# Kernel optimization log

Hardware: AMD Instinct MI355X
Metric: run time of the kernel (lower is better)

Reference implementation:

```python
import jax, jax.numpy as jnp
import numpy as np

EMBED_DIM = 1024
NUM_HEADS = 16
HEAD_DIM = EMBED_DIM // NUM_HEADS


def setup_inputs() -> dict:
    key = jax.random.key(0)
    ks = jax.random.split(key, 10)
    B, S, D = 4, 2048, EMBED_DIM
    s = 1.0 / np.sqrt(D)
    return {
        "x": jax.random.normal(ks[0], (B, S, D), dtype=jnp.float32),
        "Wq": jax.random.normal(ks[1], (D, D), dtype=jnp.float32) * s,
        "bq": jnp.zeros((D,), dtype=jnp.float32),
        "Wk": jax.random.normal(ks[2], (D, D), dtype=jnp.float32) * s,
        "bk": jnp.zeros((D,), dtype=jnp.float32),
        "Wv": jax.random.normal(ks[3], (D, D), dtype=jnp.float32) * s,
        "bv": jnp.zeros((D,), dtype=jnp.float32),
        "Wo": jax.random.normal(ks[4], (D, D), dtype=jnp.float32) * s,
        "bo": jnp.zeros((D,), dtype=jnp.float32),
        "ln_w": jnp.ones((D,), dtype=jnp.float32),
        "ln_b": jnp.zeros((D,), dtype=jnp.float32),
    }


def _layernorm(x, w, b, eps=1e-5):
    mu = jnp.mean(x, axis=-1, keepdims=True)
    var = jnp.mean(jnp.square(x - mu), axis=-1, keepdims=True)
    return (x - mu) * jax.lax.rsqrt(var + eps) * w + b


def reference(x, Wq, bq, Wk, bk, Wv, bv, Wo, bo, ln_w, ln_b):
    B, S, D = x.shape
    H, hd = NUM_HEADS, HEAD_DIM
    # projections (torch Linear: x @ W.T + b)
    q = (x @ Wq.T + bq).reshape(B, S, H, hd).transpose(0, 2, 1, 3)  # [B,H,S,hd]
    k = (x @ Wk.T + bk).reshape(B, S, H, hd).transpose(0, 2, 1, 3)
    v = (x @ Wv.T + bv).reshape(B, S, H, hd).transpose(0, 2, 1, 3)
    scores = jnp.einsum("bhqd,bhkd->bhqk", q, k) / np.sqrt(hd)
    attn = jax.nn.softmax(scores, axis=-1)
    out = jnp.einsum("bhqk,bhkd->bhqd", attn, v)
    out = out.transpose(0, 2, 1, 3).reshape(B, S, D)
    out = out @ Wo.T + bo
    return _layernorm(out, ln_w, ln_b)
```

## Files before the change

### kernel.cpp

```cpp
#include <hip/hip_runtime.h>
#include <hip/hip_bf16.h>
#include <math.h>

typedef unsigned short u16;
typedef unsigned int   u32;
typedef short bf16x8 __attribute__((ext_vector_type(8)));
typedef float f32x4  __attribute__((ext_vector_type(4)));
typedef float f32x16 __attribute__((ext_vector_type(16)));
typedef u32   u32x4  __attribute__((ext_vector_type(4)));

#define B_   4
#define S_   2048
#define D_   1024
#define H_   16
#define HD_  64
#define M_   (B_*S_)

static __device__ __forceinline__ u16 f2bf(float f) {
  __hip_bfloat16 h = __float2bfloat16(f);
  return *reinterpret_cast<u16*>(&h);
}
static __device__ __forceinline__ u32 pack_bf(float lo, float hi) {
  return (u32)f2bf(lo) | ((u32)f2bf(hi) << 16);
}
static __device__ __forceinline__ u32 pack_bf_trunc(float lo, float hi) {
  return __builtin_amdgcn_perm(__float_as_uint(hi), __float_as_uint(lo), 0x07060302u);
}
static __device__ __forceinline__ f32x16 zero16() {
  f32x16 z;
#pragma unroll
  for (int i = 0; i < 16; ++i) z[i] = 0.f;
  return z;
}

typedef __attribute__((address_space(1))) const u32* gas_t;
typedef __attribute__((address_space(3))) u32* las_t;
static __device__ __forceinline__ void g2l16(const void* g, void* l) {
  __builtin_amdgcn_global_load_lds((gas_t)g, (las_t)l, 16, 0, 0);
}

__global__ __launch_bounds__(256) void cast_kernel(const float* __restrict__ in,
                                                   u16* __restrict__ out, int n) {
  int i = (blockIdx.x * 256 + threadIdx.x) * 4;
  if (i >= n) return;
  float4 v = *reinterpret_cast<const float4*>(in + i);
  out[i + 0] = f2bf(v.x);
  out[i + 1] = f2bf(v.y);
  out[i + 2] = f2bf(v.z);
  out[i + 3] = f2bf(v.w);
}

__global__ __launch_bounds__(256) void gemm_qkv(const u16* __restrict__ A,
                                                const u16* __restrict__ Wq,
                                                const u16* __restrict__ Wk,
                                                const u16* __restrict__ Wv,
                                                const float* __restrict__ bq,
                                                const float* __restrict__ bk,
                                                const float* __restrict__ bv,
                                                u16* __restrict__ Qo,
                                                u16* __restrict__ Ko,
                                                u16* __restrict__ Vo) {
  const int tid  = threadIdx.x;
  const int lane = tid & 63;
  const int wave = tid >> 6;
  const int m16  = lane & 15;
  const int quad = lane >> 4;
  const int wm   = wave & 1;
  const int wn   = wave >> 1;
  const int which = blockIdx.x % 3;
  const int m0   = (blockIdx.x / 3) * 128;
  const int n0   = blockIdx.y * 128;

  const u16* W = which == 0 ? Wq : which == 1 ? Wk : Wv;
  const float* bias = which == 0 ? bq : which == 1 ? bk : bv;

  __shared__ __align__(16) u16 As[128 * 32];
  __shared__ __align__(16) u16 Bs[128 * 32];

  f32x4 acc[4][4];
#pragma unroll
  for (int i = 0; i < 4; ++i)
#pragma unroll
    for (int j = 0; j < 4; ++j) acc[i][j] = (f32x4){0.f, 0.f, 0.f, 0.f};

  for (int k0 = 0; k0 < 1024; k0 += 32) {
#pragma unroll
    for (int i = 0; i < 2; ++i) {
      int e0  = i * 256 + (wave << 6);
      int e   = e0 + lane;
      int row = e >> 2;
      int c8  = (e & 3) * 8;
      g2l16(&A[(size_t)(m0 + row) * 1024 + k0 + c8], &As[e0 * 8]);
      g2l16(&W[(size_t)(n0 + row) * 1024 + k0 + c8], &Bs[e0 * 8]);
    }
    __syncthreads();

    bf16x8 af[4], bfr[4];
#pragma unroll
    for (int mt = 0; mt < 4; ++mt)
      af[mt] = *reinterpret_cast<const bf16x8*>(&As[(wm * 64 + mt * 16 + m16) * 32 + quad * 8]);
#pragma unroll
    for (int nt = 0; nt < 4; ++nt)
      bfr[nt] = *reinterpret_cast<const bf16x8*>(&Bs[(wn * 64 + nt * 16 + m16) * 32 + quad * 8]);

#pragma unroll
    for (int mt = 0; mt < 4; ++mt)
#pragma unroll
      for (int nt = 0; nt < 4; ++nt)
        acc[mt][nt] = __builtin_amdgcn_mfma_f32_16x16x32_bf16(af[mt], bfr[nt], acc[mt][nt], 0, 0, 0);
    __syncthreads();
  }

  const float scale = which == 0 ? 0.125f * 1.44269504f : 1.0f;
  u16* ob = which == 0 ? Qo : which == 1 ? Ko : Vo;
#pragma unroll
  for (int mt = 0; mt < 4; ++mt) {
#pragma unroll
    for (int nt = 0; nt < 4; ++nt) {
      int col = n0 + wn * 64 + nt * 16 + m16;
      float bi = bias[col];
#pragma unroll
      for (int r = 0; r < 4; ++r) {
        int row = m0 + wm * 64 + mt * 16 + quad * 4 + r;
        float v = (acc[mt][nt][r] + bi) * scale;
        int b = row >> 11, s = row & 2047;
        int h = col >> 6,  d = col & 63;
        if (which < 2)
          ob[(size_t)((b * H_ + h) * S_ + s) * HD_ + d] = f2bf(v);
        else
          ob[(size_t)((b * H_ + h) * HD_ + d) * S_ + s] = f2bf(v);
      }
    }
  }
}

__global__ __launch_bounds__(256) void gemm_bt(const u16* __restrict__ A,
                                               const u16* __restrict__ W,
                                               const float* __restrict__ bias,
                                               float* __restrict__ out) {
  const int tid  = threadIdx.x;
  const int lane = tid & 63;
  const int wave = tid >> 6;
  const int m16  = lane & 15;
  const int quad = lane >> 4;
  const int wm   = wave & 1;
  const int wn   = wave >> 1;
  const int m0   = blockIdx.x * 128;
  const int n0   = blockIdx.y * 128;

  __shared__ __align__(16) u16 As[128 * 32];
  __shared__ __align__(16) u16 Bs[128 * 32];

  f32x4 acc[4][4];
#pragma unroll
  for (int i = 0; i < 4; ++i)
#pragma unroll
    for (int j = 0; j < 4; ++j) acc[i][j] = (f32x4){0.f, 0.f, 0.f, 0.f};

  for (int k0 = 0; k0 < 1024; k0 += 32) {
#pragma unroll
    for (int i = 0; i < 2; ++i) {
      int e0  = i * 256 + (wave << 6);
      int e   = e0 + lane;
      int row = e >> 2;
      int c8  = (e & 3) * 8;
      g2l16(&A[(size_t)(m0 + row) * 1024 + k0 + c8], &As[e0 * 8]);
      g2l16(&W[(size_t)(n0 + row) * 1024 + k0 + c8], &Bs[e0 * 8]);
    }
    __syncthreads();

    bf16x8 af[4], bfr[4];
#pragma unroll
    for (int mt = 0; mt < 4; ++mt)
      af[mt] = *reinterpret_cast<const bf16x8*>(&As[(wm * 64 + mt * 16 + m16) * 32 + quad * 8]);
#pragma unroll
    for (int nt = 0; nt < 4; ++nt)
      bfr[nt] = *reinterpret_cast<const bf16x8*>(&Bs[(wn * 64 + nt * 16 + m16) * 32 + quad * 8]);

#pragma unroll
    for (int mt = 0; mt < 4; ++mt)
#pragma unroll
      for (int nt = 0; nt < 4; ++nt)
        acc[mt][nt] = __builtin_amdgcn_mfma_f32_16x16x32_bf16(af[mt], bfr[nt], acc[mt][nt], 0, 0, 0);
    __syncthreads();
  }

#pragma unroll
  for (int mt = 0; mt < 4; ++mt) {
#pragma unroll
    for (int nt = 0; nt < 4; ++nt) {
      int col = n0 + wn * 64 + nt * 16 + m16;
      float bi = bias[col];
#pragma unroll
      for (int r = 0; r < 4; ++r) {
        int row = m0 + wm * 64 + mt * 16 + quad * 4 + r;
        out[(size_t)row * 1024 + col] = acc[mt][nt][r] + bi;
      }
    }
  }
}

__global__ __launch_bounds__(256, 4) void attn_kernel(const u16* __restrict__ Q,
                                                      const u16* __restrict__ K,
                                                      const u16* __restrict__ Vt,
                                                      u16* __restrict__ out) {
  const int tid  = threadIdx.x;
  const int lane = tid & 63;
  const int wave = tid >> 6;
  const int r32  = lane & 31;
  const int h32  = lane >> 5;
  const int bh   = blockIdx.y;
  const int q0   = blockIdx.x * 128 + wave * 32;

  __shared__ __align__(16) u16 Ks[64 * 72];
  __shared__ __align__(16) u16 Vs[64 * 72];

  bf16x8 qf[4];
  {
    const u16* qbase = Q + (size_t)(bh * S_ + q0 + r32) * HD_ + h32 * 8;
#pragma unroll
    for (int dc = 0; dc < 4; ++dc)
      qf[dc] = *reinterpret_cast<const bf16x8*>(qbase + dc * 16);
  }

  f32x16 acc[2];
#pragma unroll
  for (int dt = 0; dt < 2; ++dt) acc[dt] = zero16();
  float lsum = 0.f;

  for (int kt = 0; kt < S_ / 64; ++kt) {
    const int k0 = kt * 64;
#pragma unroll
    for (int i = 0; i < 2; ++i) {
      int e   = tid + i * 256;
      int row = e >> 3;
      int c8  = (e & 7) * 8;
      *reinterpret_cast<uint4*>(&Ks[row * 72 + c8]) =
          *reinterpret_cast<const uint4*>(&K[(size_t)(bh * S_ + k0 + row) * HD_ + c8]);
      *reinterpret_cast<uint4*>(&Vs[row * 72 + c8]) =
          *reinterpret_cast<const uint4*>(&Vt[(size_t)(bh * HD_ + row) * S_ + k0 + c8]);
    }
    __syncthreads();

    f32x16 sc[2];
#pragma unroll
    for (int nt = 0; nt < 2; ++nt) {
      sc[nt] = zero16();
#pragma unroll
      for (int dc = 0; dc < 4; ++dc) {
        bf16x8 kf = *reinterpret_cast<const bf16x8*>(&Ks[(nt * 32 + r32) * 72 + dc * 16 + h32 * 8]);
        sc[nt] = __builtin_amdgcn_mfma_f32_32x32x16_bf16(kf, qf[dc], sc[nt], 0, 0, 0);
      }
    }

    u32 pk[2][8];
    float ps = 0.f;
#pragma unroll
    for (int nt = 0; nt < 2; ++nt)
#pragma unroll
      for (int i = 0; i < 8; ++i) {
        float p0 = __builtin_amdgcn_exp2f(sc[nt][2 * i]);
        float p1 = __builtin_amdgcn_exp2f(sc[nt][2 * i + 1]);
        ps += p0 + p1;
        pk[nt][i] = pack_bf_trunc(p0, p1);
      }
    lsum += ps;

#pragma unroll
    for (int nt = 0; nt < 2; ++nt) {
#pragma unroll
      for (int kc2 = 0; kc2 < 2; ++kc2) {
        u32 s0 = h32 ? pk[nt][4 * kc2 + 0] : pk[nt][4 * kc2 + 2];
        u32 s1 = h32 ? pk[nt][4 * kc2 + 1] : pk[nt][4 * kc2 + 3];
        u32 x0 = (u32)__shfl_xor((int)s0, 32);
        u32 x1 = (u32)__shfl_xor((int)s1, 32);
        u32x4 bw;
        bw[0] = h32 ? x0 : pk[nt][4 * kc2 + 0];
        bw[1] = h32 ? x1 : pk[nt][4 * kc2 + 1];
        bw[2] = h32 ? pk[nt][4 * kc2 + 2] : x0;
        bw[3] = h32 ? pk[nt][4 * kc2 + 3] : x1;
        bf16x8 pfrag = *reinterpret_cast<bf16x8*>(&bw);
        const int kc = nt * 2 + kc2;
#pragma unroll
        for (int dt = 0; dt < 2; ++dt) {
          bf16x8 vf = *reinterpret_cast<const bf16x8*>(&Vs[(dt * 32 + r32) * 72 + kc * 16 + h32 * 8]);
          acc[dt] = __builtin_amdgcn_mfma_f32_32x32x16_bf16(vf, pfrag, acc[dt], 0, 0, 0);
        }
      }
    }
    __syncthreads();
  }

  const int b = bh >> 4, hh = bh & 15;
  float lt  = lsum + __shfl_xor(lsum, 32);
  float inv = 1.f / lt;
  int srow = q0 + r32;
  u16* orow = out + (size_t)(b * S_ + srow) * D_ + hh * HD_;
#pragma unroll
  for (int dt = 0; dt < 2; ++dt) {
#pragma unroll
    for (int g = 0; g < 4; ++g) {
      uint2 w;
      w.x = pack_bf(acc[dt][4 * g + 0] * inv, acc[dt][4 * g + 1] * inv);
      w.y = pack_bf(acc[dt][4 * g + 2] * inv, acc[dt][4 * g + 3] * inv);
      *reinterpret_cast<uint2*>(orow + dt * 32 + 8 * g + 4 * h32) = w;
    }
  }
}

__global__ __launch_bounds__(256) void ln_kernel(const float* __restrict__ X,
                                                 const float* __restrict__ w,
                                                 const float* __restrict__ b,
                                                 float* __restrict__ out) {
  const int row = blockIdx.x;
  const int tid = threadIdx.x;
  const float* x = X + (size_t)row * 1024;
  float vals[4];
  float s = 0.f, s2 = 0.f;
#pragma unroll
  for (int i = 0; i < 4; ++i) {
    float v = x[tid + i * 256];
    vals[i] = v;
    s += v;
    s2 += v * v;
  }
#pragma unroll
  for (int off = 32; off; off >>= 1) {
    s  += __shfl_xor(s, off);
    s2 += __shfl_xor(s2, off);
  }
  __shared__ float a1[4], a2[4];
  if ((tid & 63) == 0) { a1[tid >> 6] = s; a2[tid >> 6] = s2; }
  __syncthreads();
  s  = a1[0] + a1[1] + a1[2] + a1[3];
  s2 = a2[0] + a2[1] + a2[2] + a2[3];
  float mu  = s * (1.f / 1024.f);
  float var = s2 * (1.f / 1024.f) - mu * mu;
  float inv = rsqrtf(var + 1e-5f);
#pragma unroll
  for (int i = 0; i < 4; ++i) {
    int c = tid + i * 256;
    out[(size_t)row * 1024 + c] = (vals[i] - mu) * inv * w[c] + b[c];
  }
}

extern "C" void kernel_launch(void* const* d_in, const int* in_sizes, int n_in,
                              void* d_out, int out_size, void* d_ws, size_t ws_size,
                              hipStream_t stream) {
  const float* x   = (const float*)d_in[0];
  const float* Wq  = (const float*)d_in[1];
  const float* bq  = (const float*)d_in[2];
  const float* Wk  = (const float*)d_in[3];
  const float* bk  = (const float*)d_in[4];
  const float* Wv  = (const float*)d_in[5];
  const float* bv  = (const float*)d_in[6];
  const float* Wo  = (const float*)d_in[7];
  const float* bo  = (const float*)d_in[8];
  const float* lnw = (const float*)d_in[9];
  const float* lnb = (const float*)d_in[10];

  const size_t MB = 1024ull * 1024ull;
  char* ws = (char*)d_ws;
  u16* xb  = (u16*)(ws + 0);
  u16* Qb  = (u16*)(ws + 16 * MB);
  u16* Kb  = (u16*)(ws + 32 * MB);
  u16* Vtb = (u16*)(ws + 48 * MB);
  u16* Wqb = (u16*)(ws + 64 * MB);
  u16* Wkb = (u16*)(ws + 66 * MB);
  u16* Wvb = (u16*)(ws + 68 * MB);
  u16* Wob = (u16*)(ws + 70 * MB);
  float* Of = (float*)(ws + 16 * MB);

  cast_kernel<<<(M_ * D_) / 1024, 256, 0, stream>>>(x, xb, M_ * D_);
  cast_kernel<<<(D_ * D_) / 1024, 256, 0, stream>>>(Wq, Wqb, D_ * D_);
  cast_kernel<<<(D_ * D_) / 1024, 256, 0, stream>>>(Wk, Wkb, D_ * D_);
  cast_kernel<<<(D_ * D_) / 1024, 256, 0, stream>>>(Wv, Wvb, D_ * D_);
  cast_kernel<<<(D_ * D_) / 1024, 256, 0, stream>>>(Wo, Wob, D_ * D_);

  gemm_qkv<<<dim3((M_ / 128) * 3, D_ / 128), 256, 0, stream>>>(
      xb, Wqb, Wkb, Wvb, bq, bk, bv, Qb, Kb, Vtb);

  attn_kernel<<<dim3(S_ / 128, B_ * H_), 256, 0, stream>>>(Qb, Kb, Vtb, xb);

  gemm_bt<<<dim3(M_ / 128, D_ / 128), 256, 0, stream>>>(xb, Wob, bo, Of);

  ln_kernel<<<M_, 256, 0, stream>>>(Of, lnw, lnb, (float*)d_out);
}
```

Baseline: 335.0 us.

## Fuse cast kernels, vectorize V-transpose stores, register-prefetch K/V tiles in attention

Merges the five fp32-to-bf16 cast launches into one kernel that writes packed 8-byte stores. In the QKV GEMM epilogue, the four consecutive-sequence bf16 values for the transposed V output are packed into one 8-byte store instead of four scalar stores. The attention kernel now prefetches the next K/V tile into registers while computing on the current LDS tile, which hides global latency at the cost of extra registers under a 4-block occupancy bound.

Result: faster. 303.9 us (-9.3%).

```diff
diff --git a/kernel.cpp b/kernel.cpp
--- a/kernel.cpp
+++ b/kernel.cpp
@@ -39,15 +39,35 @@
   __builtin_amdgcn_global_load_lds((gas_t)g, (las_t)l, 16, 0, 0);
 }
 
-__global__ __launch_bounds__(256) void cast_kernel(const float* __restrict__ in,
-                                                   u16* __restrict__ out, int n) {
-  int i = (blockIdx.x * 256 + threadIdx.x) * 4;
-  if (i >= n) return;
-  float4 v = *reinterpret_cast<const float4*>(in + i);
-  out[i + 0] = f2bf(v.x);
-  out[i + 1] = f2bf(v.y);
-  out[i + 2] = f2bf(v.z);
-  out[i + 3] = f2bf(v.w);
+__global__ __launch_bounds__(256) void cast_all(const float* __restrict__ x,
+                                                const float* __restrict__ Wq,
+                                                const float* __restrict__ Wk,
+                                                const float* __restrict__ Wv,
+                                                const float* __restrict__ Wo,
+                                                u16* __restrict__ xb,
+                                                u16* __restrict__ Wqb,
+                                                u16* __restrict__ Wkb,
+                                                u16* __restrict__ Wvb,
+                                                u16* __restrict__ Wob) {
+  int bid = blockIdx.x;
+  const float* src;
+  u16* dst;
+  int off;
+  if (bid < 8192) {
+    src = x; dst = xb; off = bid;
+  } else {
+    int t = bid - 8192;
+    int w = t >> 10;
+    off   = t & 1023;
+    src = w == 0 ? Wq : w == 1 ? Wk : w == 2 ? Wv : Wo;
+    dst = w == 0 ? Wqb : w == 1 ? Wkb : w == 2 ? Wvb : Wob;
+  }
+  int i = (off * 256 + threadIdx.x) * 4;
+  float4 v = *reinterpret_cast<const float4*>(src + i);
+  uint2 o;
+  o.x = pack_bf(v.x, v.y);
+  o.y = pack_bf(v.z, v.w);
+  *reinterpret_cast<uint2*>(dst + i) = o;
 }
 
 __global__ __launch_bounds__(256) void gemm_qkv(const u16* __restrict__ A,
@@ -119,16 +139,21 @@
     for (int nt = 0; nt < 4; ++nt) {
       int col = n0 + wn * 64 + nt * 16 + m16;
       float bi = bias[col];
-#pragma unroll
-      for (int r = 0; r < 4; ++r) {
-        int row = m0 + wm * 64 + mt * 16 + quad * 4 + r;
-        float v = (acc[mt][nt][r] + bi) * scale;
-        int b = row >> 11, s = row & 2047;
-        int h = col >> 6,  d = col & 63;
-        if (which < 2)
-          ob[(size_t)((b * H_ + h) * S_ + s) * HD_ + d] = f2bf(v);
-        else
-          ob[(size_t)((b * H_ + h) * HD_ + d) * S_ + s] = f2bf(v);
+      int row0 = m0 + wm * 64 + mt * 16 + quad * 4;
+      int b = row0 >> 11, s = row0 & 2047;
+      int h = col >> 6,  d = col & 63;
+      float v[4];
+#pragma unroll
+      for (int r = 0; r < 4; ++r) v[r] = (acc[mt][nt][r] + bi) * scale;
+      if (which < 2) {
+#pragma unroll
+        for (int r = 0; r < 4; ++r)
+          ob[(size_t)((b * H_ + h) * S_ + s + r) * HD_ + d] = f2bf(v[r]);
+      } else {
+        uint2 w;
+        w.x = pack_bf(v[0], v[1]);
+        w.y = pack_bf(v[2], v[3]);
+        *reinterpret_cast<uint2*>(&ob[(size_t)((b * H_ + h) * HD_ + d) * S_ + s]) = w;
       }
     }
   }
@@ -215,6 +240,13 @@
   __shared__ __align__(16) u16 Ks[64 * 72];
   __shared__ __align__(16) u16 Vs[64 * 72];
 
+  const u16* kbase = K  + (size_t)bh * S_ * HD_;
+  const u16* vbase = Vt + (size_t)bh * HD_ * S_;
+  const int e  = tid;
+  const int e2 = tid + 256;
+  const int row_a = e >> 3,  c8_a = (e & 7) * 8;
+  const int row_b = e2 >> 3, c8_b = (e2 & 7) * 8;
+
   bf16x8 qf[4];
   {
     const u16* qbase = Q + (size_t)(bh * S_ + q0 + r32) * HD_ + h32 * 8;
@@ -228,19 +260,26 @@
   for (int dt = 0; dt < 2; ++dt) acc[dt] = zero16();
   float lsum = 0.f;
 
-  for (int kt = 0; kt < S_ / 64; ++kt) {
-    const int k0 = kt * 64;
-#pragma unroll
-    for (int i = 0; i < 2; ++i) {
-      int e   = tid + i * 256;
-      int row = e >> 3;
-      int c8  = (e & 7) * 8;
-      *reinterpret_cast<uint4*>(&Ks[row * 72 + c8]) =
-          *reinterpret_cast<const uint4*>(&K[(size_t)(bh * S_ + k0 + row) * HD_ + c8]);
-      *reinterpret_cast<uint4*>(&Vs[row * 72 + c8]) =
-          *reinterpret_cast<const uint4*>(&Vt[(size_t)(bh * HD_ + row) * S_ + k0 + c8]);
-    }
-    __syncthreads();
+  uint4 kr0 = *reinterpret_cast<const uint4*>(&kbase[(size_t)row_a * HD_ + c8_a]);
+  uint4 kr1 = *reinterpret_cast<const uint4*>(&kbase[(size_t)row_b * HD_ + c8_b]);
+  uint4 vr0 = *reinterpret_cast<const uint4*>(&vbase[(size_t)row_a * S_ + c8_a]);
+  uint4 vr1 = *reinterpret_cast<const uint4*>(&vbase[(size_t)row_b * S_ + c8_b]);
+
+  const int NT = S_ / 64;
+  for (int kt = 0; kt < NT; ++kt) {
+    *reinterpret_cast<uint4*>(&Ks[row_a * 72 + c8_a]) = kr0;
+    *reinterpret_cast<uint4*>(&Ks[row_b * 72 + c8_b]) = kr1;
+    *reinterpret_cast<uint4*>(&Vs[row_a * 72 + c8_a]) = vr0;
+    *reinterpret_cast<uint4*>(&Vs[row_b * 72 + c8_b]) = vr1;
+    __syncthreads();
+
+    {
+      const int kn = (kt + 1 < NT ? kt + 1 : kt) * 64;
+      kr0 = *reinterpret_cast<const uint4*>(&kbase[(size_t)(kn + row_a) * HD_ + c8_a]);
+      kr1 = *reinterpret_cast<const uint4*>(&kbase[(size_t)(kn + row_b) * HD_ + c8_b]);
+      vr0 = *reinterpret_cast<const uint4*>(&vbase[(size_t)row_a * S_ + kn + c8_a]);
+      vr1 = *reinterpret_cast<const uint4*>(&vbase[(size_t)row_b * S_ + kn + c8_b]);
+    }
 
     f32x16 sc[2];
 #pragma unroll
@@ -371,11 +410,7 @@
   u16* Wob = (u16*)(ws + 70 * MB);
   float* Of = (float*)(ws + 16 * MB);
 
-  cast_kernel<<<(M_ * D_) / 1024, 256, 0, stream>>>(x, xb, M_ * D_);
-  cast_kernel<<<(D_ * D_) / 1024, 256, 0, stream>>>(Wq, Wqb, D_ * D_);
-  cast_kernel<<<(D_ * D_) / 1024, 256, 0, stream>>>(Wk, Wkb, D_ * D_);
-  cast_kernel<<<(D_ * D_) / 1024, 256, 0, stream>>>(Wv, Wvb, D_ * D_);
-  cast_kernel<<<(D_ * D_) / 1024, 256, 0, stream>>>(Wo, Wob, D_ * D_);
+  cast_all<<<8192 + 4096, 256, 0, stream>>>(x, Wq, Wk, Wv, Wo, xb, Wqb, Wkb, Wvb, Wob);
 
   gemm_qkv<<<dim3((M_ / 128) * 3, D_ / 128), 256, 0, stream>>>(
       xb, Wqb, Wkb, Wvb, bq, bk, bv, Qb, Kb, Vtb);
```
